# Kernel optimization log

Hardware: AMD Instinct MI355X
Metric: run time of the kernel (lower is better)

The kernel has to match this reference:

```python
import jax, jax.numpy as jnp
import numpy as np

B, S, H, V = 256, 15, 512, 50257

def setup_inputs() -> dict:
    key = jax.random.key(0)
    ks = jax.random.split(key, 12)
    sc_h = 1.0 / np.sqrt(H)
    sc_in = 1.0 / np.sqrt(2 * H)
    return {
        "input_tokens": jax.random.randint(ks[0], (B, 1), 0, V),
        "hidden": jax.random.normal(ks[1], (1, B, H), jnp.float32),
        "encoder_outputs": jax.random.normal(ks[2], (B, S, H), jnp.float32),
        "emb_table": jax.random.normal(ks[3], (V, H), jnp.float32),
        "attn_W": jax.random.uniform(ks[4], (H, H), jnp.float32, -sc_h, sc_h),
        "attn_b": jax.random.uniform(ks[5], (H,), jnp.float32, -sc_h, sc_h),
        "W_ih": jax.random.uniform(ks[6], (3 * H, 2 * H), jnp.float32, -sc_in, sc_in),
        "W_hh": jax.random.uniform(ks[7], (3 * H, H), jnp.float32, -sc_h, sc_h),
        "b_ih": jax.random.uniform(ks[8], (3 * H,), jnp.float32, -sc_h, sc_h),
        "b_hh": jax.random.uniform(ks[9], (3 * H,), jnp.float32, -sc_h, sc_h),
        "out_W": jax.random.uniform(ks[10], (V, H), jnp.float32, -sc_h, sc_h),
        "out_b": jax.random.uniform(ks[11], (V,), jnp.float32, -sc_h, sc_h),
    }


def reference(input_tokens, hidden, encoder_outputs, emb_table, attn_W, attn_b,
              W_ih, W_hh, b_ih, b_hh, out_W, out_b):
    # Embedding (dropout is identity in eval/reference mode): [B,1,H]
    embedded = emb_table[input_tokens]
    h = hidden[0]  # [B,H]

    # Bahdanau-style scores, vectorized over the seq dim instead of the python loop:
    # energies[b,s] = attn(enc[b,s]);  score[b,s] = <h[b], energies[b,s]>
    energies = jnp.einsum("bsh,oh->bso", encoder_outputs, attn_W) + attn_b  # [B,S,H]
    attn_scores = jnp.einsum("bso,bo->bs", energies, h)                      # [B,S]
    attn_weights = jax.nn.softmax(attn_scores, axis=1)                       # [B,S]

    # context = weights @ encoder_outputs: [B,1,H]
    context = jnp.einsum("bs,bsh->bh", attn_weights, encoder_outputs)[:, None, :]

    # GRU single step (PyTorch gate order: r, z, n)
    x = jnp.concatenate([embedded, context], axis=2)[:, 0]  # [B,2H]
    gi = x @ W_ih.T + b_ih   # [B,3H]
    gh = h @ W_hh.T + b_hh   # [B,3H]
    i_r, i_z, i_n = jnp.split(gi, 3, axis=1)
    h_r, h_z, h_n = jnp.split(gh, 3, axis=1)
    r = jax.nn.sigmoid(i_r + h_r)
    z = jax.nn.sigmoid(i_z + h_z)
    n = jnp.tanh(i_n + r * h_n)
    h_new = (1.0 - z) * n + z * h            # [B,H]

    logits = h_new[:, None, :] @ out_W.T + out_b   # [B,1,V]
    log_probs = jax.nn.log_softmax(logits, axis=-1)
    return log_probs, h_new[None], attn_weights
```

## Files before the change

kernel.cpp:

```cpp
#include <hip/hip_runtime.h>

#define V_SIZE 50257
#define B_SIZE 256
#define S_LEN  15
#define H_DIM  512

typedef __attribute__((ext_vector_type(8))) short bf16x8;
typedef __attribute__((ext_vector_type(4))) float f32x4;

__device__ __forceinline__ unsigned short f2bf(float f) {
    unsigned int u = __float_as_uint(f);
    u += 0x7fffu + ((u >> 16) & 1u);
    return (unsigned short)(u >> 16);
}

__global__ __launch_bounds__(256) void u_kernel(
    const float* __restrict__ hidden, const float* __restrict__ attn_W,
    float* __restrict__ u)
{
    __shared__ float h_s[16][H_DIM];
    const int tid = threadIdx.x;
    const int b0 = blockIdx.y * 16, n0 = blockIdx.x * 32;
    const float4* hv = (const float4*)(hidden + (size_t)b0 * H_DIM);
    float4* hs4 = (float4*)&h_s[0][0];
    #pragma unroll
    for (int i = 0; i < 8; ++i) hs4[tid + i * 256] = hv[tid + i * 256];
    __syncthreads();
    const int n = n0 + (tid & 31);
    const int m = (tid >> 5) * 2;
    float a0 = 0.f, a1 = 0.f;
    #pragma unroll 8
    for (int o = 0; o < H_DIM; ++o) {
        float w = attn_W[(size_t)o * H_DIM + n];
        a0 += h_s[m][o] * w;
        a1 += h_s[m + 1][o] * w;
    }
    u[(size_t)(b0 + m) * H_DIM + n] = a0;
    u[(size_t)(b0 + m + 1) * H_DIM + n] = a1;
}

__global__ __launch_bounds__(256) void attn_kernel(
    const float* __restrict__ hidden, const float* __restrict__ enc,
    const float* __restrict__ u, const int* __restrict__ tokens,
    const float* __restrict__ emb, float* __restrict__ attnw_out,
    unsigned short* __restrict__ x_bf, unsigned short* __restrict__ h_bf)
{
    const int b = blockIdx.x, tid = threadIdx.x;
    __shared__ float u_s[H_DIM];
    __shared__ float sc_s[S_LEN];
    __shared__ float w_s[S_LEN];
    u_s[tid]       = u[(size_t)b * H_DIM + tid];
    u_s[tid + 256] = u[(size_t)b * H_DIM + tid + 256];
    h_bf[(size_t)b * H_DIM + tid]       = f2bf(hidden[(size_t)b * H_DIM + tid]);
    h_bf[(size_t)b * H_DIM + tid + 256] = f2bf(hidden[(size_t)b * H_DIM + tid + 256]);
    const int tok = tokens[b];
    x_bf[(size_t)b * 2 * H_DIM + tid]       = f2bf(emb[(size_t)tok * H_DIM + tid]);
    x_bf[(size_t)b * 2 * H_DIM + tid + 256] = f2bf(emb[(size_t)tok * H_DIM + tid + 256]);
    __syncthreads();
    const int wave = tid >> 6, lane = tid & 63;
    for (int s = wave; s < S_LEN; s += 4) {
        const float* e = enc + ((size_t)b * S_LEN + s) * H_DIM;
        float acc = 0.f;
        #pragma unroll
        for (int k = 0; k < H_DIM / 64; ++k) acc += e[lane + k * 64] * u_s[lane + k * 64];
        #pragma unroll
        for (int off = 32; off; off >>= 1) acc += __shfl_down(acc, off);
        if (lane == 0) sc_s[s] = acc;
    }
    __syncthreads();
    float mx = -1e30f;
    for (int s = 0; s < S_LEN; ++s) mx = fmaxf(mx, sc_s[s]);
    float sum = 0.f;
    for (int s = 0; s < S_LEN; ++s) sum += __expf(sc_s[s] - mx);
    const float inv = 1.f / sum;
    if (tid < S_LEN) {
        float w = __expf(sc_s[tid] - mx) * inv;
        w_s[tid] = w;
        attnw_out[b * S_LEN + tid] = w;
    }
    __syncthreads();
    #pragma unroll
    for (int hh = 0; hh < 2; ++hh) {
        int h = tid + hh * 256;
        float c = 0.f;
        #pragma unroll
        for (int s = 0; s < S_LEN; ++s)
            c += w_s[s] * enc[((size_t)b * S_LEN + s) * H_DIM + h];
        x_bf[(size_t)b * 2 * H_DIM + H_DIM + h] = f2bf(c);
    }
}

struct GemmP {
    const unsigned short* A; const float* B; const float* bias; float* C;
    int N; int K;
};

template<int BM, int BN, int BK, int WR, int WC>
__global__ __launch_bounds__(256) void gemm_nt(GemmP p0, GemmP p1)
{
    GemmP p = (blockIdx.z == 0) ? p0 : p1;
    constexpr int LDA = BK + 8;
    __shared__ __align__(16) unsigned short As[BM][LDA];
    __shared__ __align__(16) unsigned short Bs[BN][LDA];
    const int tid = threadIdx.x;
    const int bn0 = blockIdx.x * BN;
    const int bm0 = blockIdx.y * BM;
    const int wave = tid >> 6, lane = tid & 63;
    const int wm = (wave / WC) * (BM / WR);
    const int wn = (wave % WC) * (BN / WC);
    constexpr int MF = BM / WR / 16, NF = BN / WC / 16;
    const int n16 = lane & 15, quad = lane >> 4;

    f32x4 acc[MF][NF] = {};

    for (int k0 = 0; k0 < p.K; k0 += BK) {
        #pragma unroll
        for (int it = 0; it < BM / 32; ++it) {
            int v = it * 256 + tid;
            int row = v >> 3, seg = v & 7;
            *(uint4*)&As[row][seg * 8] =
                *(const uint4*)(p.A + (size_t)(bm0 + row) * p.K + k0 + seg * 8);
        }
        #pragma unroll
        for (int it = 0; it < BN / 32; ++it) {
            int v = it * 256 + tid;
            int row = v >> 3, seg = v & 7;
            int gv = bn0 + row;
            float4 w0 = make_float4(0, 0, 0, 0), w1 = make_float4(0, 0, 0, 0);
            if (gv < p.N) {
                const float4* src = (const float4*)(p.B + (size_t)gv * p.K + k0 + seg * 8);
                w0 = src[0]; w1 = src[1];
            }
            uint4 pk;
            pk.x = (unsigned)f2bf(w0.x) | ((unsigned)f2bf(w0.y) << 16);
            pk.y = (unsigned)f2bf(w0.z) | ((unsigned)f2bf(w0.w) << 16);
            pk.z = (unsigned)f2bf(w1.x) | ((unsigned)f2bf(w1.y) << 16);
            pk.w = (unsigned)f2bf(w1.z) | ((unsigned)f2bf(w1.w) << 16);
            *(uint4*)&Bs[row][seg * 8] = pk;
        }
        __syncthreads();
        #pragma unroll
        for (int kk = 0; kk < BK; kk += 32) {
            bf16x8 af[MF], bfr[NF];
            #pragma unroll
            for (int i = 0; i < MF; ++i)
                af[i] = *(const bf16x8*)&As[wm + i * 16 + n16][kk + quad * 8];
            #pragma unroll
            for (int j = 0; j < NF; ++j)
                bfr[j] = *(const bf16x8*)&Bs[wn + j * 16 + n16][kk + quad * 8];
            #pragma unroll
            for (int i = 0; i < MF; ++i)
                #pragma unroll
                for (int j = 0; j < NF; ++j)
                    acc[i][j] = __builtin_amdgcn_mfma_f32_16x16x32_bf16(
                        af[i], bfr[j], acc[i][j], 0, 0, 0);
        }
        __syncthreads();
    }
    #pragma unroll
    for (int i = 0; i < MF; ++i) {
        const int r0 = bm0 + wm + i * 16 + quad * 4;
        #pragma unroll
        for (int j = 0; j < NF; ++j) {
            const int c = bn0 + wn + j * 16 + n16;
            if (c < p.N) {
                const float bv = p.bias[c];
                #pragma unroll
                for (int r = 0; r < 4; ++r)
                    p.C[(size_t)(r0 + r) * p.N + c] = acc[i][j][r] + bv;
            }
        }
    }
}

__global__ __launch_bounds__(256) void gru_kernel(
    const float* __restrict__ gi, const float* __restrict__ gh,
    const float* __restrict__ hidden, float* __restrict__ hnew_out,
    unsigned short* __restrict__ hnew_bf)
{
    const int idx = blockIdx.x * 256 + threadIdx.x;
    const int b = idx >> 9, h = idx & 511;
    const float* gib = gi + (size_t)b * 3 * H_DIM;
    const float* ghb = gh + (size_t)b * 3 * H_DIM;
    float r = 1.f / (1.f + __expf(-(gib[h] + ghb[h])));
    float z = 1.f / (1.f + __expf(-(gib[H_DIM + h] + ghb[H_DIM + h])));
    float n = gib[2 * H_DIM + h] + r * ghb[2 * H_DIM + h];
    n = 1.f - 2.f / (1.f + __expf(2.f * n));
    float hp = hidden[idx];
    float hn = (1.f - z) * n + z * hp;
    hnew_out[idx] = hn;
    hnew_bf[idx] = f2bf(hn);
}

__global__ __launch_bounds__(1024) void logsoftmax_kernel(float* __restrict__ logits)
{
    const int b = blockIdx.x, tid = threadIdx.x;
    float* row = logits + (size_t)b * V_SIZE;
    float m = -1e30f, s = 0.f;
    for (int c = tid; c < V_SIZE; c += 1024) {
        float x = row[c];
        float nm = fmaxf(m, x);
        s = s * __expf(m - nm) + __expf(x - nm);
        m = nm;
    }
    const int lane = tid & 63, wave = tid >> 6;
    #pragma unroll
    for (int off = 32; off; off >>= 1) {
        float m2 = __shfl_down(m, off), s2 = __shfl_down(s, off);
        float nm = fmaxf(m, m2);
        s = s * __expf(m - nm) + s2 * __expf(m2 - nm);
        m = nm;
    }
    __shared__ float msh[16], ssh[16], lse_sh;
    if (lane == 0) { msh[wave] = m; ssh[wave] = s; }
    __syncthreads();
    if (tid == 0) {
        float M = msh[0], S = ssh[0];
        for (int w = 1; w < 16; ++w) {
            float nm = fmaxf(M, msh[w]);
            S = S * __expf(M - nm) + ssh[w] * __expf(msh[w] - nm);
            M = nm;
        }
        lse_sh = M + logf(S);
    }
    __syncthreads();
    const float lse = lse_sh;
    for (int c = tid; c < V_SIZE; c += 1024) row[c] -= lse;
}

constexpr size_t OFF_U      = 0;
constexpr size_t OFF_XBF    = 524288;
constexpr size_t OFF_HBF    = 1048576;
constexpr size_t OFF_HNEWBF = 1310720;
constexpr size_t OFF_GI     = 1572864;
constexpr size_t OFF_GH     = 3145728;

extern "C" void kernel_launch(void* const* d_in, const int* in_sizes, int n_in,
                              void* d_out, int out_size, void* d_ws, size_t ws_size,
                              hipStream_t stream) {
    const int*   tokens = (const int*)d_in[0];
    const float* hidden = (const float*)d_in[1];
    const float* enc    = (const float*)d_in[2];
    const float* emb    = (const float*)d_in[3];
    const float* attn_W = (const float*)d_in[4];
    const float* W_ih   = (const float*)d_in[6];
    const float* W_hh   = (const float*)d_in[7];
    const float* b_ih   = (const float*)d_in[8];
    const float* b_hh   = (const float*)d_in[9];
    const float* out_W  = (const float*)d_in[10];
    const float* out_b  = (const float*)d_in[11];

    float* out = (float*)d_out;
    float* logp      = out;
    float* hnew_out  = out + (size_t)B_SIZE * V_SIZE;
    float* attnw_out = hnew_out + (size_t)B_SIZE * H_DIM;

    char* ws = (char*)d_ws;
    float*          u_ws    = (float*)(ws + OFF_U);
    unsigned short* x_bf    = (unsigned short*)(ws + OFF_XBF);
    unsigned short* h_bf    = (unsigned short*)(ws + OFF_HBF);
    unsigned short* hnew_bf = (unsigned short*)(ws + OFF_HNEWBF);
    float*          gi_ws   = (float*)(ws + OFF_GI);
    float*          gh_ws   = (float*)(ws + OFF_GH);

    u_kernel<<<dim3(16, 16), 256, 0, stream>>>(hidden, attn_W, u_ws);
    attn_kernel<<<dim3(256), 256, 0, stream>>>(hidden, enc, u_ws, tokens, emb,
                                               attnw_out, x_bf, h_bf);
    GemmP gi_p { x_bf, W_ih, b_ih, gi_ws, 3 * H_DIM, 2 * H_DIM };
    GemmP gh_p { h_bf, W_hh, b_hh, gh_ws, 3 * H_DIM, H_DIM };
    gemm_nt<64, 64, 64, 2, 2><<<dim3(24, 4, 2), 256, 0, stream>>>(gi_p, gh_p);
    gru_kernel<<<dim3(512), 256, 0, stream>>>(gi_ws, gh_ws, hidden, hnew_out, hnew_bf);
    GemmP lg { hnew_bf, out_W, out_b, logp, V_SIZE, H_DIM };
    gemm_nt<256, 64, 64, 4, 1><<<dim3((V_SIZE + 63) / 64, 1, 1), 256, 0, stream>>>(lg, lg);
    logsoftmax_kernel<<<dim3(256), 1024, 0, stream>>>(logp);
}
```

Before: 375.4 us.

## Fuse partial log-softmax stats into logits GEMM and register-prefetch tiles

The logits GEMM epilogue now computes per-row partial max and sum-exp for each 64-column block and writes them to workspace. A new finalize kernel merges these partials and subtracts the LSE with vectorized stores, so the full-row read pass of the old log-softmax is no longer needed. The GEMM also prefetches the next K tile into registers while computing the current one, with BK reduced to 32 and LDS padding changed. This adds workspace use and a fallback path when the workspace is too small.

```diff
diff --git a/kernel.cpp b/kernel.cpp
--- a/kernel.cpp
+++ b/kernel.cpp
@@ -4,6 +4,7 @@
 #define B_SIZE 256
 #define S_LEN  15
 #define H_DIM  512
+#define NBLK_LG 786
 
 typedef __attribute__((ext_vector_type(8))) short bf16x8;
 typedef __attribute__((ext_vector_type(4))) float f32x4;
@@ -92,14 +93,14 @@
 
 struct GemmP {
     const unsigned short* A; const float* B; const float* bias; float* C;
-    int N; int K;
+    int N; int K; float* pm; float* ps;
 };
 
-template<int BM, int BN, int BK, int WR, int WC>
+template<int BM, int BN, int BK, int WR, int WC, bool PART>
 __global__ __launch_bounds__(256) void gemm_nt(GemmP p0, GemmP p1)
 {
     GemmP p = (blockIdx.z == 0) ? p0 : p1;
-    constexpr int LDA = BK + 8;
+    constexpr int LDA = BK + 24;
     __shared__ __align__(16) unsigned short As[BM][LDA];
     __shared__ __align__(16) unsigned short Bs[BN][LDA];
     const int tid = threadIdx.x;
@@ -110,35 +111,62 @@
     const int wn = (wave % WC) * (BN / WC);
     constexpr int MF = BM / WR / 16, NF = BN / WC / 16;
     const int n16 = lane & 15, quad = lane >> 4;
-
-    f32x4 acc[MF][NF] = {};
-
-    for (int k0 = 0; k0 < p.K; k0 += BK) {
-        #pragma unroll
-        for (int it = 0; it < BM / 32; ++it) {
+    constexpr int SEG = BK / 8;
+    constexpr int IA = BM * SEG / 256;
+    constexpr int IB = BN * SEG / 256;
+    static_assert(IA >= 1 && IB >= 1, "tile too small");
+
+    uint4 ra[IA];
+    float4 rb0[IB], rb1[IB];
+
+    auto loadA = [&](int k0) {
+        #pragma unroll
+        for (int it = 0; it < IA; ++it) {
             int v = it * 256 + tid;
-            int row = v >> 3, seg = v & 7;
-            *(uint4*)&As[row][seg * 8] =
-                *(const uint4*)(p.A + (size_t)(bm0 + row) * p.K + k0 + seg * 8);
-        }
-        #pragma unroll
-        for (int it = 0; it < BN / 32; ++it) {
+            int row = v / SEG, seg = v % SEG;
+            ra[it] = *(const uint4*)(p.A + (size_t)(bm0 + row) * p.K + k0 + seg * 8);
+        }
+    };
+    auto loadB = [&](int k0) {
+        #pragma unroll
+        for (int it = 0; it < IB; ++it) {
             int v = it * 256 + tid;
-            int row = v >> 3, seg = v & 7;
+            int row = v / SEG, seg = v % SEG;
             int gv = bn0 + row;
-            float4 w0 = make_float4(0, 0, 0, 0), w1 = make_float4(0, 0, 0, 0);
+            float4 z; z.x = z.y = z.z = z.w = 0.f;
+            rb0[it] = z; rb1[it] = z;
             if (gv < p.N) {
                 const float4* src = (const float4*)(p.B + (size_t)gv * p.K + k0 + seg * 8);
-                w0 = src[0]; w1 = src[1];
+                rb0[it] = src[0]; rb1[it] = src[1];
             }
+        }
+    };
+    auto storeAB = [&]() {
+        #pragma unroll
+        for (int it = 0; it < IA; ++it) {
+            int v = it * 256 + tid;
+            int row = v / SEG, seg = v % SEG;
+            *(uint4*)&As[row][seg * 8] = ra[it];
+        }
+        #pragma unroll
+        for (int it = 0; it < IB; ++it) {
+            int v = it * 256 + tid;
+            int row = v / SEG, seg = v % SEG;
             uint4 pk;
-            pk.x = (unsigned)f2bf(w0.x) | ((unsigned)f2bf(w0.y) << 16);
-            pk.y = (unsigned)f2bf(w0.z) | ((unsigned)f2bf(w0.w) << 16);
-            pk.z = (unsigned)f2bf(w1.x) | ((unsigned)f2bf(w1.y) << 16);
-            pk.w = (unsigned)f2bf(w1.z) | ((unsigned)f2bf(w1.w) << 16);
+            pk.x = (unsigned)f2bf(rb0[it].x) | ((unsigned)f2bf(rb0[it].y) << 16);
+            pk.y = (unsigned)f2bf(rb0[it].z) | ((unsigned)f2bf(rb0[it].w) << 16);
+            pk.z = (unsigned)f2bf(rb1[it].x) | ((unsigned)f2bf(rb1[it].y) << 16);
+            pk.w = (unsigned)f2bf(rb1[it].z) | ((unsigned)f2bf(rb1[it].w) << 16);
             *(uint4*)&Bs[row][seg * 8] = pk;
         }
+    };
+
+    f32x4 acc[MF][NF] = {};
+    loadA(0); loadB(0);
+    for (int k0 = 0; k0 < p.K; k0 += BK) {
+        storeAB();
         __syncthreads();
+        if (k0 + BK < p.K) { loadA(k0 + BK); loadB(k0 + BK); }
         #pragma unroll
         for (int kk = 0; kk < BK; kk += 32) {
             bf16x8 af[MF], bfr[NF];
@@ -157,18 +185,44 @@
         }
         __syncthreads();
     }
+
+    int cj[NF]; float bvv[NF]; bool okj[NF];
+    #pragma unroll
+    for (int j = 0; j < NF; ++j) {
+        cj[j] = bn0 + wn + j * 16 + n16;
+        okj[j] = cj[j] < p.N;
+        bvv[j] = okj[j] ? p.bias[cj[j]] : 0.f;
+    }
     #pragma unroll
     for (int i = 0; i < MF; ++i) {
         const int r0 = bm0 + wm + i * 16 + quad * 4;
-        #pragma unroll
-        for (int j = 0; j < NF; ++j) {
-            const int c = bn0 + wn + j * 16 + n16;
-            if (c < p.N) {
-                const float bv = p.bias[c];
-                #pragma unroll
-                for (int r = 0; r < 4; ++r)
-                    p.C[(size_t)(r0 + r) * p.N + c] = acc[i][j][r] + bv;
+        if (PART) {
+            #pragma unroll
+            for (int r = 0; r < 4; ++r) {
+                float m = -1e30f;
+                #pragma unroll
+                for (int j = 0; j < NF; ++j)
+                    if (okj[j]) m = fmaxf(m, acc[i][j][r] + bvv[j]);
+                #pragma unroll
+                for (int d = 1; d < 16; d <<= 1) m = fmaxf(m, __shfl_xor(m, d));
+                float s = 0.f;
+                #pragma unroll
+                for (int j = 0; j < NF; ++j)
+                    if (okj[j]) s += __expf(acc[i][j][r] + bvv[j] - m);
+                #pragma unroll
+                for (int d = 1; d < 16; d <<= 1) s += __shfl_xor(s, d);
+                if (n16 == 0) {
+                    int row = r0 + r;
+                    p.pm[(size_t)row * NBLK_LG + blockIdx.x] = m;
+                    p.ps[(size_t)row * NBLK_LG + blockIdx.x] = s;
+                }
             }
+        }
+        #pragma unroll
+        for (int j = 0; j < NF; ++j) if (okj[j]) {
+            #pragma unroll
+            for (int r = 0; r < 4; ++r)
+                p.C[(size_t)(r0 + r) * p.N + cj[j]] = acc[i][j][r] + bvv[j];
         }
     }
 }
@@ -192,6 +246,54 @@
     hnew_bf[idx] = f2bf(hn);
 }
 
+__global__ __launch_bounds__(1024) void finalize_kernel(
+    float* __restrict__ logits, const float* __restrict__ pm,
+    const float* __restrict__ ps)
+{
+    const int b = blockIdx.x, tid = threadIdx.x;
+    float m = -1e30f, s = 0.f;
+    for (int i = tid; i < NBLK_LG; i += 1024) {
+        float mm = pm[(size_t)b * NBLK_LG + i], ss = ps[(size_t)b * NBLK_LG + i];
+        float nm = fmaxf(m, mm);
+        s = s * __expf(m - nm) + ss * __expf(mm - nm);
+        m = nm;
+    }
+    const int lane = tid & 63, wave = tid >> 6;
+    #pragma unroll
+    for (int off = 32; off; off >>= 1) {
+        float m2 = __shfl_down(m, off), s2 = __shfl_down(s, off);
+        float nm = fmaxf(m, m2);
+        s = s * __expf(m - nm) + s2 * __expf(m2 - nm);
+        m = nm;
+    }
+    __shared__ float msh[16], ssh[16], lse_sh;
+    if (lane == 0) { msh[wave] = m; ssh[wave] = s; }
+    __syncthreads();
+    if (tid == 0) {
+        float M = msh[0], S = ssh[0];
+        for (int w = 1; w < 16; ++w) {
+            float nm = fmaxf(M, msh[w]);
+            S = S * __expf(M - nm) + ssh[w] * __expf(msh[w] - nm);
+            M = nm;
+        }
+        lse_sh = M + logf(S);
+    }
+    __syncthreads();
+    const float lse = lse_sh;
+    float* row = logits + (size_t)b * V_SIZE;
+    const int pre = (4 - (b & 3)) & 3;
+    if ((int)tid < pre) row[tid] -= lse;
+    const int nv = (V_SIZE - pre) >> 2;
+    float4* r4 = (float4*)(row + pre);
+    for (int i = tid; i < nv; i += 1024) {
+        float4 v = r4[i];
+        v.x -= lse; v.y -= lse; v.z -= lse; v.w -= lse;
+        r4[i] = v;
+    }
+    const int ts = pre + nv * 4;
+    if (ts + (int)tid < V_SIZE) row[ts + tid] -= lse;
+}
+
 __global__ __launch_bounds__(1024) void logsoftmax_kernel(float* __restrict__ logits)
 {
     const int b = blockIdx.x, tid = threadIdx.x;
@@ -234,6 +336,9 @@
 constexpr size_t OFF_HNEWBF = 1310720;
 constexpr size_t OFF_GI     = 1572864;
 constexpr size_t OFF_GH     = 3145728;
+constexpr size_t OFF_PM     = 4718592;
+constexpr size_t OFF_PS     = 5523456;
+constexpr size_t WS_NEED    = 6328320;
 
 extern "C" void kernel_launch(void* const* d_in, const int* in_sizes, int n_in,
                               void* d_out, int out_size, void* d_ws, size_t ws_size,
@@ -262,15 +367,24 @@
     unsigned short* hnew_bf = (unsigned short*)(ws + OFF_HNEWBF);
     float*          gi_ws   = (float*)(ws + OFF_GI);
     float*          gh_ws   = (float*)(ws + OFF_GH);
+    float*          pm_ws   = (float*)(ws + OFF_PM);
+    float*          ps_ws   = (float*)(ws + OFF_PS);
 
     u_kernel<<<dim3(16, 16), 256, 0, stream>>>(hidden, attn_W, u_ws);
     attn_kernel<<<dim3(256), 256, 0, stream>>>(hidden, enc, u_ws, tokens, emb,
                                                attnw_out, x_bf, h_bf);
-    GemmP gi_p { x_bf, W_ih, b_ih, gi_ws, 3 * H_DIM, 2 * H_DIM };
-    GemmP gh_p { h_bf, W_hh, b_hh, gh_ws, 3 * H_DIM, H_DIM };
-    gemm_nt<64, 64, 64, 2, 2><<<dim3(24, 4, 2), 256, 0, stream>>>(gi_p, gh_p);
+    GemmP gi_p { x_bf, W_ih, b_ih, gi_ws, 3 * H_DIM, 2 * H_DIM, nullptr, nullptr };
+    GemmP gh_p { h_bf, W_hh, b_hh, gh_ws, 3 * H_DIM, H_DIM, nullptr, nullptr };
+    gemm_nt<64, 64, 32, 2, 2, false><<<dim3(24, 4, 2), 256, 0, stream>>>(gi_p, gh_p);
     gru_kernel<<<dim3(512), 256, 0, stream>>>(gi_ws, gh_ws, hidden, hnew_out, hnew_bf);
-    GemmP lg { hnew_bf, out_W, out_b, logp, V_SIZE, H_DIM };
-    gemm_nt<256, 64, 64, 4, 1><<<dim3((V_SIZE + 63) / 64, 1, 1), 256, 0, stream>>>(lg, lg);
-    logsoftmax_kernel<<<dim3(256), 1024, 0, stream>>>(logp);
-}
+
+    if (ws_size >= WS_NEED) {
+        GemmP lg { hnew_bf, out_W, out_b, logp, V_SIZE, H_DIM, pm_ws, ps_ws };
+        gemm_nt<256, 64, 32, 4, 1, true><<<dim3(NBLK_LG, 1, 1), 256, 0, stream>>>(lg, lg);
+        finalize_kernel<<<dim3(256), 1024, 0, stream>>>(logp, pm_ws, ps_ws);
+    } else {
+        GemmP lg { hnew_bf, out_W, out_b, logp, V_SIZE, H_DIM, nullptr, nullptr };
+        gemm_nt<256, 64, 32, 4, 1, false><<<dim3(NBLK_LG, 1, 1), 256, 0, stream>>>(lg, lg);
+        logsoftmax_kernel<<<dim3(256), 1024, 0, stream>>>(logp);
+    }
+}
```

Result: slower. 415.8 us (+10.8%).

## Fuse partial log-softmax stats into logits GEMM and add finalize pass

Applied to the files above, without the earlier changes.

Replaces the generic logits GEMM with a dedicated kernel that reads A directly from global memory, uses a larger K tile, and writes per-block row max and sum-of-exp partials from the epilogue. A finalize kernel merges the 786 partials per row and subtracts the log-sum-exp across a 2D grid. This removes the full re-read of the 51MB logits matrix that the old log-softmax needed to compute its statistics. It needs extra workspace and falls back to the old path when the workspace is too small.

```diff
diff --git a/kernel.cpp b/kernel.cpp
--- a/kernel.cpp
+++ b/kernel.cpp
@@ -4,6 +4,7 @@
 #define B_SIZE 256
 #define S_LEN  15
 #define H_DIM  512
+#define NBLK_LG 786
 
 typedef __attribute__((ext_vector_type(8))) short bf16x8;
 typedef __attribute__((ext_vector_type(4))) float f32x4;
@@ -173,6 +174,104 @@
     }
 }
 
+template<bool PART>
+__global__ __launch_bounds__(256, 4) void gemm_lg(
+    const unsigned short* __restrict__ A, const float* __restrict__ B,
+    const float* __restrict__ bias, float* __restrict__ C,
+    float* __restrict__ pm, float* __restrict__ ps)
+{
+    constexpr int BN = 64, BK = 128;
+    constexpr int LDB = BK + 8;
+    __shared__ __align__(16) unsigned short Bs[BN][LDB];
+    const int tid = threadIdx.x;
+    const int bn0 = blockIdx.x * BN;
+    const int wave = tid >> 6, lane = tid & 63;
+    const int wm = wave * 64;
+    const int n16 = lane & 15, quad = lane >> 4;
+
+    f32x4 acc[4][4] = {};
+    const unsigned short* arow[4];
+    #pragma unroll
+    for (int i = 0; i < 4; ++i) arow[i] = A + (size_t)(wm + i * 16 + n16) * H_DIM;
+
+    for (int k0 = 0; k0 < H_DIM; k0 += BK) {
+        #pragma unroll
+        for (int it = 0; it < 4; ++it) {
+            int v = it * 256 + tid;
+            int row = v >> 4, seg = v & 15;
+            int gv = bn0 + row;
+            float4 w0 = make_float4(0, 0, 0, 0), w1 = make_float4(0, 0, 0, 0);
+            if (gv < V_SIZE) {
+                const float4* src = (const float4*)(B + (size_t)gv * H_DIM + k0 + seg * 8);
+                w0 = src[0]; w1 = src[1];
+            }
+            uint4 pk;
+            pk.x = (unsigned)f2bf(w0.x) | ((unsigned)f2bf(w0.y) << 16);
+            pk.y = (unsigned)f2bf(w0.z) | ((unsigned)f2bf(w0.w) << 16);
+            pk.z = (unsigned)f2bf(w1.x) | ((unsigned)f2bf(w1.y) << 16);
+            pk.w = (unsigned)f2bf(w1.z) | ((unsigned)f2bf(w1.w) << 16);
+            *(uint4*)&Bs[row][seg * 8] = pk;
+        }
+        __syncthreads();
+        #pragma unroll
+        for (int kk = 0; kk < BK; kk += 32) {
+            bf16x8 af[4], bfr[4];
+            #pragma unroll
+            for (int i = 0; i < 4; ++i)
+                af[i] = *(const bf16x8*)(arow[i] + k0 + kk + quad * 8);
+            #pragma unroll
+            for (int j = 0; j < 4; ++j)
+                bfr[j] = *(const bf16x8*)&Bs[j * 16 + n16][kk + quad * 8];
+            #pragma unroll
+            for (int i = 0; i < 4; ++i)
+                #pragma unroll
+                for (int j = 0; j < 4; ++j)
+                    acc[i][j] = __builtin_amdgcn_mfma_f32_16x16x32_bf16(
+                        af[i], bfr[j], acc[i][j], 0, 0, 0);
+        }
+        __syncthreads();
+    }
+
+    int cj[4]; float bvv[4]; bool okj[4];
+    #pragma unroll
+    for (int j = 0; j < 4; ++j) {
+        cj[j] = bn0 + j * 16 + n16;
+        okj[j] = cj[j] < V_SIZE;
+        bvv[j] = okj[j] ? bias[cj[j]] : 0.f;
+    }
+    #pragma unroll
+    for (int i = 0; i < 4; ++i) {
+        const int r0 = wm + i * 16 + quad * 4;
+        if (PART) {
+            #pragma unroll
+            for (int r = 0; r < 4; ++r) {
+                float m = -1e30f;
+                #pragma unroll
+                for (int j = 0; j < 4; ++j)
+                    if (okj[j]) m = fmaxf(m, acc[i][j][r] + bvv[j]);
+                #pragma unroll
+                for (int d = 1; d < 16; d <<= 1) m = fmaxf(m, __shfl_xor(m, d));
+                float s = 0.f;
+                #pragma unroll
+                for (int j = 0; j < 4; ++j)
+                    if (okj[j]) s += __expf(acc[i][j][r] + bvv[j] - m);
+                #pragma unroll
+                for (int d = 1; d < 16; d <<= 1) s += __shfl_xor(s, d);
+                if (n16 == 0) {
+                    pm[(size_t)blockIdx.x * B_SIZE + r0 + r] = m;
+                    ps[(size_t)blockIdx.x * B_SIZE + r0 + r] = s;
+                }
+            }
+        }
+        #pragma unroll
+        for (int j = 0; j < 4; ++j) if (okj[j]) {
+            #pragma unroll
+            for (int r = 0; r < 4; ++r)
+                C[(size_t)(r0 + r) * V_SIZE + cj[j]] = acc[i][j][r] + bvv[j];
+        }
+    }
+}
+
 __global__ __launch_bounds__(256) void gru_kernel(
     const float* __restrict__ gi, const float* __restrict__ gh,
     const float* __restrict__ hidden, float* __restrict__ hnew_out,
@@ -192,6 +291,47 @@
     hnew_bf[idx] = f2bf(hn);
 }
 
+__global__ __launch_bounds__(1024) void finalize_kernel(
+    float* __restrict__ logits, const float* __restrict__ pm,
+    const float* __restrict__ ps)
+{
+    const int b = blockIdx.x, tid = threadIdx.x;
+    float m = -1e30f, s = 0.f;
+    for (int i = tid; i < NBLK_LG; i += 1024) {
+        float mm = pm[(size_t)i * B_SIZE + b], ss = ps[(size_t)i * B_SIZE + b];
+        float nm = fmaxf(m, mm);
+        s = s * __expf(m - nm) + ss * __expf(mm - nm);
+        m = nm;
+    }
+    const int lane = tid & 63, wave = tid >> 6;
+    #pragma unroll
+    for (int off = 32; off; off >>= 1) {
+        float m2 = __shfl_down(m, off), s2 = __shfl_down(s, off);
+        float nm = fmaxf(m, m2);
+        s = s * __expf(m - nm) + s2 * __expf(m2 - nm);
+        m = nm;
+    }
+    __shared__ float msh[16], ssh[16], lse_sh;
+    if (lane == 0) { msh[wave] = m; ssh[wave] = s; }
+    __syncthreads();
+    if (tid == 0) {
+        float M = msh[0], S = ssh[0];
+        for (int w = 1; w < 16; ++w) {
+            float nm = fmaxf(M, msh[w]);
+            S = S * __expf(M - nm) + ssh[w] * __expf(msh[w] - nm);
+            M = nm;
+        }
+        lse_sh = M + logf(S);
+    }
+    __syncthreads();
+    const float lse = lse_sh;
+    constexpr int HALF = (V_SIZE + 1) / 2;
+    const int start = blockIdx.y * HALF;
+    const int end = min(V_SIZE, start + HALF);
+    float* row = logits + (size_t)b * V_SIZE;
+    for (int c = start + tid; c < end; c += 1024) row[c] -= lse;
+}
+
 __global__ __launch_bounds__(1024) void logsoftmax_kernel(float* __restrict__ logits)
 {
     const int b = blockIdx.x, tid = threadIdx.x;
@@ -234,6 +374,9 @@
 constexpr size_t OFF_HNEWBF = 1310720;
 constexpr size_t OFF_GI     = 1572864;
 constexpr size_t OFF_GH     = 3145728;
+constexpr size_t OFF_PM     = 4718592;
+constexpr size_t OFF_PS     = 5523456;
+constexpr size_t WS_NEED    = 6328320;
 
 extern "C" void kernel_launch(void* const* d_in, const int* in_sizes, int n_in,
                               void* d_out, int out_size, void* d_ws, size_t ws_size,
@@ -262,6 +405,8 @@
     unsigned short* hnew_bf = (unsigned short*)(ws + OFF_HNEWBF);
     float*          gi_ws   = (float*)(ws + OFF_GI);
     float*          gh_ws   = (float*)(ws + OFF_GH);
+    float*          pm_ws   = (float*)(ws + OFF_PM);
+    float*          ps_ws   = (float*)(ws + OFF_PS);
 
     u_kernel<<<dim3(16, 16), 256, 0, stream>>>(hidden, attn_W, u_ws);
     attn_kernel<<<dim3(256), 256, 0, stream>>>(hidden, enc, u_ws, tokens, emb,
@@ -270,7 +415,14 @@
     GemmP gh_p { h_bf, W_hh, b_hh, gh_ws, 3 * H_DIM, H_DIM };
     gemm_nt<64, 64, 64, 2, 2><<<dim3(24, 4, 2), 256, 0, stream>>>(gi_p, gh_p);
     gru_kernel<<<dim3(512), 256, 0, stream>>>(gi_ws, gh_ws, hidden, hnew_out, hnew_bf);
-    GemmP lg { hnew_bf, out_W, out_b, logp, V_SIZE, H_DIM };
-    gemm_nt<256, 64, 64, 4, 1><<<dim3((V_SIZE + 63) / 64, 1, 1), 256, 0, stream>>>(lg, lg);
-    logsoftmax_kernel<<<dim3(256), 1024, 0, stream>>>(logp);
-}
+
+    if (ws_size >= WS_NEED) {
+        gemm_lg<true><<<dim3(NBLK_LG), 256, 0, stream>>>(
+            hnew_bf, out_W, out_b, logp, pm_ws, ps_ws);
+        finalize_kernel<<<dim3(256, 2), 1024, 0, stream>>>(logp, pm_ws, ps_ws);
+    } else {
+        gemm_lg<false><<<dim3(NBLK_LG), 256, 0, stream>>>(
+            hnew_bf, out_W, out_b, logp, nullptr, nullptr);
+        logsoftmax_kernel<<<dim3(256), 1024, 0, stream>>>(logp);
+    }
+}
```

Result: no change. 372.9 us (-0.7%).
